# Kernel optimization log

Hardware: AMD Instinct MI355X
Metric: run time of the kernel (lower is better)

## Reference

```python
import jax, jax.numpy as jnp
import numpy as np

MARGIN1 = 0.3
MARGIN2 = 0.3
NUM_HARD_NEG = 10
CENTER_W = 0.01
NUM_CLASSES = 288
FEAT_DIM = 2048
N = 2048


def setup_inputs() -> dict:
    key = jax.random.key(0)
    k1, k2, k3 = jax.random.split(key, 3)
    embeddings = jax.random.normal(k1, (N, FEAT_DIM), dtype=jnp.float32)
    labels = jax.random.randint(k2, (N,), 0, NUM_CLASSES, dtype=jnp.int64)
    centers = jax.random.normal(k3, (NUM_CLASSES, FEAT_DIM), dtype=jnp.float32)
    return {"embeddings": embeddings, "labels": labels, "centers": centers}


def _pairwise_dist(x):
    # torch.cdist(x, x, p=2): Euclidean distance matrix [n, n]
    sq = jnp.sum(x * x, axis=1)
    d2 = sq[:, None] + sq[None, :] - 2.0 * (x @ x.T)
    return jnp.sqrt(jnp.maximum(d2, 1e-12))


def _quadruplet_loss(embeddings, centers, labels):
    n = embeddings.shape[0]
    dist = _pairwise_dist(embeddings)                      # [n, n]
    same = labels[:, None] == labels[None, :]
    eye = jnp.eye(n, dtype=bool)
    pos_mask = same & ~eye                                 # [n, n]
    neg_mask = ~same                                       # [n, n]

    # random positive per anchor (uniform over positives), fixed key
    u = jax.random.uniform(jax.random.key(42), (n, n))
    pos_idx = jnp.argmax(jnp.where(pos_mask, u, -1.0), axis=1)   # [n]
    has_pos = jnp.any(pos_mask, axis=1)
    neg_count = jnp.sum(neg_mask, axis=1)
    anchor_valid = has_pos & (neg_count >= 2)              # [n]

    # hard-negative mining: k smallest distances among negatives
    inf = jnp.asarray(jnp.inf, dist.dtype)
    masked = jnp.where(neg_mask, dist, inf)
    neg_d, negs1 = jax.lax.top_k(-masked, NUM_HARD_NEG)    # [n, k]
    d_an = -neg_d                                          # [n, k]

    # neg2: nearest negative (w.r.t. anchor's label set) to neg1, excluding neg1
    rows = dist[negs1]                                     # [n, k, n]
    excl = jnp.arange(n)[None, None, :] == negs1[:, :, None]
    cand = neg_mask[:, None, :] & ~excl                    # [n, k, n]
    d_n1n2 = jnp.min(jnp.where(cand, rows, inf), axis=2)   # [n, k]

    d_ap = dist[jnp.arange(n), pos_idx][:, None]           # [n, 1]

    valid = anchor_valid[:, None] & jnp.isfinite(d_an) & jnp.isfinite(d_n1n2)
    terms = (jax.nn.relu(d_ap - d_an + MARGIN1)
             + jax.nn.relu(d_ap - d_n1n2 + MARGIN2))       # [n, k]
    cnt = jnp.sum(valid)
    total = jnp.sum(jnp.where(valid, terms, 0.0))
    quad = jnp.where(cnt > 0, total / jnp.maximum(cnt, 1).astype(terms.dtype), 0.0)

    # center loss
    batch_centers = centers[labels]                        # [n, d]
    center = jnp.mean(jnp.sum((embeddings - batch_centers) ** 2, axis=1))
    return quad + CENTER_W * center


def reference(embeddings, labels, centers):
    return _quadruplet_loss(embeddings, centers, labels)
```

## Files before the change

kernel.cpp:

```cpp
#include <hip/hip_runtime.h>
#include <hip/hip_bf16.h>

#define N 2048
#define FEAT 2048
#define K_NEG 10
#define NCLS 288
#define M1 0.3f
#define M2 0.3f
#define CW 0.01f

#define BT 64
#define GT (N / BT)
#define NBLK (GT * (GT + 1) / 2)
#define BK 128
#define NT (FEAT / BK)

typedef __attribute__((ext_vector_type(8))) __bf16 bf16x8;
typedef __attribute__((ext_vector_type(4))) float f32x4;
typedef unsigned long long u64;

__device__ __forceinline__ unsigned short f32_to_bf16(float f) {
    unsigned int u = __float_as_uint(f);
    u += 0x7fffu + ((u >> 16) & 1u);
    return (unsigned short)(u >> 16);
}

__device__ __forceinline__ unsigned int rotl32(unsigned int x, int d) {
    return (x << d) | (x >> (32 - d));
}

__device__ __attribute__((noinline)) float threefry_uniform(unsigned int f) {
    const unsigned int H = (unsigned int)(N) * (unsigned int)(N) / 2u;
    unsigned int x0, x1; int word;
    if (f < H) { x0 = f;     x1 = f + H; word = 0; }
    else       { x0 = f - H; x1 = f;     word = 1; }
    unsigned int ks[3];
    ks[0] = 0u; ks[1] = 42u; ks[2] = 0u ^ 42u ^ 0x1BD11BDAu;
    x0 += ks[0]; x1 += ks[1];
    const int rotA[4] = {13, 15, 26, 6};
    const int rotB[4] = {17, 29, 16, 24};
    #pragma unroll
    for (int i = 0; i < 5; ++i) {
        const int* r = (i & 1) ? rotB : rotA;
        #pragma unroll
        for (int j = 0; j < 4; ++j) {
            x0 += x1; x1 = rotl32(x1, r[j]); x1 ^= x0;
        }
        x0 += ks[(i + 1) % 3];
        x1 += ks[(i + 2) % 3] + (unsigned int)(i + 1);
    }
    unsigned int bits = (word == 0) ? x0 : x1;
    return __uint_as_float((bits >> 9) | 0x3f800000u) - 1.0f;
}

__device__ __forceinline__ void gld16(const unsigned short* g, unsigned short* l) {
    __builtin_amdgcn_global_load_lds(
        (const __attribute__((address_space(1))) unsigned int*)g,
        (__attribute__((address_space(3))) unsigned int*)l,
        16, 0, 0);
}

__device__ __forceinline__ u64 shfl_xor_u64(u64 v, int mask) {
    unsigned int lo = (unsigned int)v, hi = (unsigned int)(v >> 32);
    lo = __shfl_xor(lo, mask);
    hi = __shfl_xor(hi, mask);
    return ((u64)hi << 32) | (u64)lo;
}

__global__ void __launch_bounds__(256) prep_kernel(
        const float* __restrict__ emb, const int* __restrict__ labels,
        const float* __restrict__ centers, unsigned short* __restrict__ xbf,
        float* __restrict__ sq, float* __restrict__ centerp) {
    int i = blockIdx.x;
    int t = threadIdx.x;
    int lab = labels[i];
    const float4* erow = (const float4*)(emb + (size_t)i * FEAT);
    const float4* crow = (const float4*)(centers + (size_t)lab * FEAT);
    uint2* xrow = (uint2*)(xbf + (size_t)i * FEAT);
    float ssum = 0.f, csum = 0.f;
    #pragma unroll
    for (int p = 0; p < 2; ++p) {
        int idx4 = p * 256 + t;
        float4 e = erow[idx4];
        float4 c = crow[idx4];
        ssum += e.x*e.x + e.y*e.y + e.z*e.z + e.w*e.w;
        float dx = e.x-c.x, dy = e.y-c.y, dz = e.z-c.z, dw = e.w-c.w;
        csum += dx*dx + dy*dy + dz*dz + dw*dw;
        unsigned int w0 = (unsigned int)f32_to_bf16(e.x) | ((unsigned int)f32_to_bf16(e.y) << 16);
        unsigned int w1 = (unsigned int)f32_to_bf16(e.z) | ((unsigned int)f32_to_bf16(e.w) << 16);
        xrow[idx4] = make_uint2(w0, w1);
    }
    #pragma unroll
    for (int off = 32; off; off >>= 1) {
        ssum += __shfl_xor(ssum, off);
        csum += __shfl_xor(csum, off);
    }
    __shared__ float s1[4], s2[4];
    int lane = t & 63, w = t >> 6;
    if (lane == 0) { s1[w] = ssum; s2[w] = csum; }
    __syncthreads();
    if (t == 0) {
        sq[i]      = s1[0] + s1[1] + s1[2] + s1[3];
        centerp[i] = s2[0] + s2[1] + s2[2] + s2[3];
    }
}

__global__ void __launch_bounds__(256) gemm_dist_kernel(
        const unsigned short* __restrict__ xbf, const float* __restrict__ sq,
        float* __restrict__ dist) {
    __shared__ __align__(16) unsigned short smem[4 * BT * BK];
    unsigned short (*As)[BT * BK] = (unsigned short(*)[BT * BK])smem;
    unsigned short (*Bs)[BT * BK] = (unsigned short(*)[BT * BK])(smem + 2 * BT * BK);
    float (*Ts)[68] = (float(*)[68])smem;

    int bid = blockIdx.x;
    int p = (bid & 7) * (NBLK / 8) + (bid >> 3);
    int by = 0, rem = p;
    while (rem >= GT - by) { rem -= GT - by; ++by; }
    int bx = by + rem;
    int brow0 = by * BT;
    int bcol0 = bx * BT;

    int t = threadIdx.x;
    int lane = t & 63, wid = t >> 6;
    int wr = wid >> 1, wc = wid & 1;
    f32x4 acc[2][2] = {};

    #define STAGE(buf, kelem) do {                                              \
        _Pragma("unroll")                                                       \
        for (int q = 0; q < 4; ++q) {                                           \
            int chunk = q * 256 + t;                                            \
            int row = chunk >> 4, c16 = chunk & 15;                             \
            int csrc = c16 ^ (row & 7);             \
            gld16(xbf + (size_t)(brow0 + row) * FEAT + (kelem) + csrc * 8,      \
                  &As[buf][chunk * 8]);                                         \
            gld16(xbf + (size_t)(bcol0 + row) * FEAT + (kelem) + csrc * 8,      \
                  &Bs[buf][chunk * 8]);                                         \
        } } while (0)

    STAGE(0, 0);

    for (int kt = 0; kt < NT; ++kt) {
        int cur = kt & 1;
        if (kt + 1 < NT) {
            STAGE(cur ^ 1, (kt + 1) * BK);
            asm volatile("s_waitcnt vmcnt(8)" ::: "memory");
        } else {
            asm volatile("s_waitcnt vmcnt(0)" ::: "memory");
        }
        __builtin_amdgcn_s_barrier();
        asm volatile("" ::: "memory");

        bf16x8 a[4][2], b[4][2];
        #pragma unroll
        for (int kk = 0; kk < 4; ++kk) {
            #pragma unroll
            for (int m = 0; m < 2; ++m) {
                int r = wr * 32 + m * 16 + (lane & 15);
                int slot = (kk * 4 + (lane >> 4)) ^ (r & 7);
                a[kk][m] = *(const bf16x8*)(&As[cur][r * BK + slot * 8]);
            }
            #pragma unroll
            for (int n = 0; n < 2; ++n) {
                int r = wc * 32 + n * 16 + (lane & 15);
                int slot = (kk * 4 + (lane >> 4)) ^ (r & 7);
                b[kk][n] = *(const bf16x8*)(&Bs[cur][r * BK + slot * 8]);
            }
        }
        #pragma unroll
        for (int m = 0; m < 2; ++m)
            #pragma unroll
            for (int n = 0; n < 2; ++n)
                #pragma unroll
                for (int kk = 0; kk < 4; ++kk)
                    acc[m][n] = __builtin_amdgcn_mfma_f32_16x16x32_bf16(a[kk][m], b[kk][n], acc[m][n], 0, 0, 0);

        asm volatile("" ::: "memory");
        __builtin_amdgcn_s_barrier();
        asm volatile("" ::: "memory");
    }
    #undef STAGE

    bool offdiag = (bx != by);
    #pragma unroll
    for (int m = 0; m < 2; ++m) {
        int lrow_base = wr * 32 + m * 16 + (lane >> 4) * 4;
        #pragma unroll
        for (int n = 0; n < 2; ++n) {
            int lcol = wc * 32 + n * 16 + (lane & 15);
            int gcol = bcol0 + lcol;
            float sqc = sq[gcol];
            #pragma unroll
            for (int r = 0; r < 4; ++r) {
                int lrow = lrow_base + r;
                int grow = brow0 + lrow;
                float d2 = sq[grow] + sqc - 2.0f * acc[m][n][r];
                float d = sqrtf(fmaxf(d2, 1e-12f));
                dist[(size_t)grow * N + gcol] = d;
                if (offdiag) Ts[lcol][lrow] = d;
            }
        }
    }
    asm volatile("s_waitcnt lgkmcnt(0)" ::: "memory");
    __builtin_amdgcn_s_barrier();
    asm volatile("" ::: "memory");
    if (offdiag) {
        int tr = t >> 2, seg = t & 3;
        float4* dst = (float4*)(dist + (size_t)(bcol0 + tr) * N + brow0 + seg * 16);
        const float* srow = &Ts[tr][seg * 16];
        #pragma unroll
        for (int x = 0; x < 4; ++x)
            dst[x] = *(const float4*)(srow + x * 4);
    }
}

__global__ void __launch_bounds__(256) topk_kernel(
        const float* __restrict__ dist, const int* __restrict__ labels,
        float* __restrict__ d_ap, int* __restrict__ avalid,
        int* __restrict__ negs1, float* __restrict__ d_an,
        float* __restrict__ rmin1, int* __restrict__ rc1, float* __restrict__ rmin2) {
    int t = threadIdx.x;
    int lane = t & 63, w = t >> 6;
    int i = blockIdx.x * 4 + w;
    int lab = labels[i];
    const float INF = __int_as_float(0x7f800000);

    __shared__ unsigned int mbuck[4][NCLS];
    for (int c = lane; c < NCLS; c += 64) mbuck[w][c] = 0x7f800000u;
    asm volatile("s_waitcnt lgkmcnt(0)" ::: "memory");

    const float4* drow = (const float4*)(dist + (size_t)i * N);
    const int4*   lrow = (const int4*)labels;

    unsigned int t0v = 0xFFFFFFFFu, t1v = 0xFFFFFFFFu, t2v = 0xFFFFFFFFu, t3v = 0xFFFFFFFFu;
    int t0j = 0, t1j = 0, t2j = 0, t3j = 0;
    float bestu = -1.0f; int bestj = 0;
    int negc = 0;

    #pragma unroll
    for (int it = 0; it < 8; ++it) {
        int idx4 = it * 64 + lane;
        float4 dv = drow[idx4];
        int4   lv = lrow[idx4];
        #pragma unroll
        for (int e = 0; e < 4; ++e) {
            float dd = (e == 0) ? dv.x : (e == 1) ? dv.y : (e == 2) ? dv.z : dv.w;
            int   lj = (e == 0) ? lv.x : (e == 1) ? lv.y : (e == 2) ? lv.z : lv.w;
            int j = idx4 * 4 + e;
            unsigned int db = __float_as_uint(dd);
            bool self = (j == i);
            if (!self && db < mbuck[w][lj]) atomicMin(&mbuck[w][lj], db);
            if (lj == lab) {
                if (!self) {
                    float u = threefry_uniform((unsigned int)(i * N + j));
                    if (u > bestu || (u == bestu && j < bestj)) { bestu = u; bestj = j; }
                }
            } else {
                negc++;
                if (db < t3v) {
                    bool lt2 = db < t2v, lt1 = db < t1v, lt0 = db < t0v;
                    t3v = lt2 ? t2v : db;   t3j = lt2 ? t2j : j;
                    unsigned int n2v = lt1 ? t1v : db; int n2j = lt1 ? t1j : j;
                    t2v = lt2 ? n2v : t2v;  t2j = lt2 ? n2j : t2j;
                    unsigned int n1v = lt0 ? t0v : db; int n1j = lt0 ? t0j : j;
                    t1v = lt1 ? n1v : t1v;  t1j = lt1 ? n1j : t1j;
                    t0v = lt0 ? db : t0v;   t0j = lt0 ? j : t0j;
                }
            }
        }
    }

    #pragma unroll
    for (int o = 1; o < 64; o <<= 1) {
        float ou = __shfl_xor(bestu, o);
        int   oj = __shfl_xor(bestj, o);
        negc += __shfl_xor(negc, o);
        if (ou > bestu || (ou == bestu && oj < bestj)) { bestu = ou; bestj = oj; }
    }
    if (lane == 0) {
        bool has_pos = (bestu >= 0.0f);
        avalid[i] = (has_pos && negc >= 2) ? 1 : 0;
        d_ap[i]   = has_pos ? dist[(size_t)i * N + bestj] : 0.0f;
    }

    #pragma unroll 1
    for (int r = 0; r < K_NEG; ++r) {
        u64 myk = ((u64)t0v << 32) | (unsigned int)t0j;
        u64 kmin = myk;
        #pragma unroll
        for (int o = 1; o < 64; o <<= 1) {
            u64 ok = shfl_xor_u64(kmin, o);
            if (ok < kmin) kmin = ok;
        }
        unsigned int hv = (unsigned int)(kmin >> 32);
        bool fin = hv < 0x7f800000u;
        if (lane == 0) {
            d_an[i * K_NEG + r]  = fin ? __uint_as_float(hv) : INF;
            negs1[i * K_NEG + r] = fin ? (int)(kmin & 0xFFFFFFFFu) : 0;
        }
        bool won = fin && (myk == kmin);
        if (won) {
            t0v = t1v; t0j = t1j; t1v = t2v; t1j = t2j; t2v = t3v; t2j = t3j;
            t3v = 0xFFFFFFFFu; t3j = 0;
        }
        if (__any(won && t0v == 0xFFFFFFFFu)) {
            if (won && t0v == 0xFFFFFFFFu) {
                u64 best = 0xFFFFFFFFFFFFFFFFull;
                #pragma unroll 1
                for (int it = 0; it < 8; ++it) {
                    int idx4 = it * 64 + lane;
                    float4 dv = drow[idx4];
                    int4   lv = lrow[idx4];
                    #pragma unroll
                    for (int e = 0; e < 4; ++e) {
                        float dd = (e == 0) ? dv.x : (e == 1) ? dv.y : (e == 2) ? dv.z : dv.w;
                        int   lj = (e == 0) ? lv.x : (e == 1) ? lv.y : (e == 2) ? lv.z : lv.w;
                        int j = idx4 * 4 + e;
                        unsigned int db = __float_as_uint(dd);
                        if (lj != lab && db < 0x7f800000u) {
                            u64 kq = ((u64)db << 32) | (unsigned int)j;
                            if (kq > myk && kq < best) best = kq;
                        }
                    }
                }
                t0v = (unsigned int)(best >> 32);
                t0j = (int)(best & 0xFFFFFFFFu);
            }
        }
    }

    asm volatile("s_waitcnt lgkmcnt(0)" ::: "memory");
    {
        float m1v = __uint_as_float(mbuck[w][lane]);
        int   c1v = lane;
        float m2v = INF;
        #pragma unroll
        for (int p = 1; p < 4; ++p) {
            float b = __uint_as_float(mbuck[w][lane + p * 64]);
            if (b < m1v) { m2v = m1v; m1v = b; c1v = lane + p * 64; }
            else         { m2v = fminf(m2v, b); }
        }
        if (lane < NCLS - 256) {
            float b = __uint_as_float(mbuck[w][lane + 256]);
            if (b < m1v) { m2v = m1v; m1v = b; c1v = lane + 256; }
            else         { m2v = fminf(m2v, b); }
        }
        #pragma unroll
        for (int o = 1; o < 64; o <<= 1) {
            float o1 = __shfl_xor(m1v, o);
            int   oc = __shfl_xor(c1v, o);
            float o2 = __shfl_xor(m2v, o);
            if (o1 < m1v) { m2v = fminf(m1v, o2); m1v = o1; c1v = oc; }
            else          { m2v = fminf(m2v, o1); }
        }
        if (lane == 0) { rmin1[i] = m1v; rc1[i] = c1v; rmin2[i] = m2v; }
    }
}

__global__ void __launch_bounds__(256) terms_kernel(
        const int* __restrict__ labels, const int* __restrict__ negs1,
        const float* __restrict__ d_an, const float* __restrict__ d_ap,
        const int* __restrict__ avalid, const float* __restrict__ rmin1,
        const int* __restrict__ rc1, const float* __restrict__ rmin2,
        float* __restrict__ terms, float* __restrict__ validf) {
    int task = blockIdx.x * 256 + threadIdx.x;
    if (task >= N * K_NEG) return;
    int i = task / K_NEG;
    int n1 = negs1[task];
    int lab = labels[i];
    const float INF = __int_as_float(0x7f800000);
    float dn2 = (rc1[n1] == lab) ? rmin2[n1] : rmin1[n1];
    float dan = d_an[task];
    float dap = d_ap[i];
    float t1 = fmaxf(dap - dan + M1, 0.0f);
    float t2 = fmaxf(dap - dn2 + M2, 0.0f);
    bool valid = (avalid[i] != 0) && (dan < INF) && (dn2 < INF);
    terms[task]  = valid ? (t1 + t2) : 0.0f;
    validf[task] = valid ? 1.0f : 0.0f;
}

__global__ void __launch_bounds__(256) finalize_kernel(
        const float* __restrict__ terms, const float* __restrict__ validf,
        const float* __restrict__ centerp, float* __restrict__ out) {
    int t = threadIdx.x;
    float ts = 0.f, vs = 0.f, cs = 0.f;
    for (int j = t * 4; j < N * K_NEG; j += 1024) {
        const float4 tv = *(const float4*)(terms + j);
        const float4 vv = *(const float4*)(validf + j);
        ts += tv.x + tv.y + tv.z + tv.w;
        vs += vv.x + vv.y + vv.z + vv.w;
    }
    for (int j = t; j < N; j += 256) cs += centerp[j];
    __shared__ float a[256], b[256], c[256];
    a[t] = ts; b[t] = vs; c[t] = cs;
    __syncthreads();
    for (int s = 128; s > 0; s >>= 1) {
        if (t < s) { a[t] += a[t + s]; b[t] += b[t + s]; c[t] += c[t + s]; }
        __syncthreads();
    }
    if (t == 0) {
        float quad = (b[0] > 0.0f) ? (a[0] / b[0]) : 0.0f;
        out[0] = quad + CW * (c[0] / (float)N);
    }
}

extern "C" void kernel_launch(void* const* d_in, const int* in_sizes, int n_in,
                              void* d_out, int out_size, void* d_ws, size_t ws_size,
                              hipStream_t stream) {
    const float* emb     = (const float*)d_in[0];
    const int*   labels  = (const int*)d_in[1];
    const float* centers = (const float*)d_in[2];
    float* out = (float*)d_out;

    char* ws = (char*)d_ws;
    unsigned short* xbf = (unsigned short*)ws;
    float* dist = (float*)(ws + (size_t)8 * 1024 * 1024);
    char* p = ws + (size_t)24 * 1024 * 1024;
    float* sq      = (float*)p; p += N * 4;
    float* centerp = (float*)p; p += N * 4;
    float* d_ap    = (float*)p; p += N * 4;
    int*   avalid  = (int*)p;   p += N * 4;
    float* rmin1   = (float*)p; p += N * 4;
    int*   rc1     = (int*)p;   p += N * 4;
    float* rmin2   = (float*)p; p += N * 4;
    int*   negs1   = (int*)p;   p += N * K_NEG * 4;
    float* d_an    = (float*)p; p += N * K_NEG * 4;
    float* terms   = (float*)p; p += N * K_NEG * 4;
    float* validf  = (float*)p; p += N * K_NEG * 4;

    prep_kernel<<<N, 256, 0, stream>>>(emb, labels, centers, xbf, sq, centerp);
    gemm_dist_kernel<<<NBLK, 256, 0, stream>>>(xbf, sq, dist);
    topk_kernel<<<N / 4, 256, 0, stream>>>(dist, labels, d_ap, avalid, negs1, d_an,
                                           rmin1, rc1, rmin2);
    terms_kernel<<<(N * K_NEG + 255) / 256, 256, 0, stream>>>(
        labels, negs1, d_an, d_ap, avalid, rmin1, rc1, rmin2, terms, validf);
    finalize_kernel<<<1, 256, 0, stream>>>(terms, validf, centerp, out);
}
```

Baseline: 68.26 us.

## Enlarge distance GEMM tile to 128x128 with two-phase transposed writeback

Raises the symmetric distance GEMM block tile from 64 to 128 and lowers the K step from 128 to 64, so each wave now accumulates a 4x4 grid of MFMA fragments. The goal is more data reuse per shared-memory load and fewer blocks. The transposed mirror write of off-diagonal tiles now goes through shared memory in two column-half phases, since the 128x128 float tile does not fit in the reused buffer at once. The cost is more accumulator registers, which may lower occupancy, and only 136 blocks, which may leave many of the 256 CUs idle.

```diff
diff --git a/kernel.cpp b/kernel.cpp
--- a/kernel.cpp
+++ b/kernel.cpp
@@ -9,10 +9,10 @@
 #define M2 0.3f
 #define CW 0.01f
 
-#define BT 64
+#define BT 128
 #define GT (N / BT)
 #define NBLK (GT * (GT + 1) / 2)
-#define BK 128
+#define BK 64
 #define NT (FEAT / BK)
 
 typedef __attribute__((ext_vector_type(8))) __bf16 bf16x8;
@@ -111,7 +111,7 @@
     __shared__ __align__(16) unsigned short smem[4 * BT * BK];
     unsigned short (*As)[BT * BK] = (unsigned short(*)[BT * BK])smem;
     unsigned short (*Bs)[BT * BK] = (unsigned short(*)[BT * BK])(smem + 2 * BT * BK);
-    float (*Ts)[68] = (float(*)[68])smem;
+    float (*Ts)[132] = (float(*)[132])smem;
 
     int bid = blockIdx.x;
     int p = (bid & 7) * (NBLK / 8) + (bid >> 3);
@@ -124,13 +124,13 @@
     int t = threadIdx.x;
     int lane = t & 63, wid = t >> 6;
     int wr = wid >> 1, wc = wid & 1;
-    f32x4 acc[2][2] = {};
+    f32x4 acc[4][4] = {};
 
     #define STAGE(buf, kelem) do {                                              \
         _Pragma("unroll")                                                       \
         for (int q = 0; q < 4; ++q) {                                           \
             int chunk = q * 256 + t;                                            \
-            int row = chunk >> 4, c16 = chunk & 15;                             \
+            int row = chunk >> 3, c16 = chunk & 7;                              \
             int csrc = c16 ^ (row & 7);             \
             gld16(xbf + (size_t)(brow0 + row) * FEAT + (kelem) + csrc * 8,      \
                   &As[buf][chunk * 8]);                                         \
@@ -151,29 +151,27 @@
         __builtin_amdgcn_s_barrier();
         asm volatile("" ::: "memory");
 
-        bf16x8 a[4][2], b[4][2];
-        #pragma unroll
-        for (int kk = 0; kk < 4; ++kk) {
+        #pragma unroll
+        for (int kk = 0; kk < 2; ++kk) {
+            bf16x8 a[4], b[4];
             #pragma unroll
-            for (int m = 0; m < 2; ++m) {
-                int r = wr * 32 + m * 16 + (lane & 15);
+            for (int m = 0; m < 4; ++m) {
+                int r = wr * 64 + m * 16 + (lane & 15);
                 int slot = (kk * 4 + (lane >> 4)) ^ (r & 7);
-                a[kk][m] = *(const bf16x8*)(&As[cur][r * BK + slot * 8]);
+                a[m] = *(const bf16x8*)(&As[cur][r * BK + slot * 8]);
             }
             #pragma unroll
-            for (int n = 0; n < 2; ++n) {
-                int r = wc * 32 + n * 16 + (lane & 15);
+            for (int n = 0; n < 4; ++n) {
+                int r = wc * 64 + n * 16 + (lane & 15);
                 int slot = (kk * 4 + (lane >> 4)) ^ (r & 7);
-                b[kk][n] = *(const bf16x8*)(&Bs[cur][r * BK + slot * 8]);
-            }
-        }
-        #pragma unroll
-        for (int m = 0; m < 2; ++m)
+                b[n] = *(const bf16x8*)(&Bs[cur][r * BK + slot * 8]);
+            }
             #pragma unroll
-            for (int n = 0; n < 2; ++n)
+            for (int m = 0; m < 4; ++m)
                 #pragma unroll
-                for (int kk = 0; kk < 4; ++kk)
-                    acc[m][n] = __builtin_amdgcn_mfma_f32_16x16x32_bf16(a[kk][m], b[kk][n], acc[m][n], 0, 0, 0);
+                for (int n = 0; n < 4; ++n)
+                    acc[m][n] = __builtin_amdgcn_mfma_f32_16x16x32_bf16(a[m], b[n], acc[m][n], 0, 0, 0);
+        }
 
         asm volatile("" ::: "memory");
         __builtin_amdgcn_s_barrier();
@@ -183,34 +181,49 @@
 
     bool offdiag = (bx != by);
     #pragma unroll
-    for (int m = 0; m < 2; ++m) {
-        int lrow_base = wr * 32 + m * 16 + (lane >> 4) * 4;
-        #pragma unroll
-        for (int n = 0; n < 2; ++n) {
-            int lcol = wc * 32 + n * 16 + (lane & 15);
-            int gcol = bcol0 + lcol;
+    for (int m = 0; m < 4; ++m) {
+        int lrow_base = wr * 64 + m * 16 + (lane >> 4) * 4;
+        #pragma unroll
+        for (int n = 0; n < 4; ++n) {
+            int gcol = bcol0 + wc * 64 + n * 16 + (lane & 15);
             float sqc = sq[gcol];
             #pragma unroll
             for (int r = 0; r < 4; ++r) {
-                int lrow = lrow_base + r;
-                int grow = brow0 + lrow;
+                int grow = brow0 + lrow_base + r;
                 float d2 = sq[grow] + sqc - 2.0f * acc[m][n][r];
                 float d = sqrtf(fmaxf(d2, 1e-12f));
                 dist[(size_t)grow * N + gcol] = d;
-                if (offdiag) Ts[lcol][lrow] = d;
-            }
-        }
-    }
-    asm volatile("s_waitcnt lgkmcnt(0)" ::: "memory");
-    __builtin_amdgcn_s_barrier();
-    asm volatile("" ::: "memory");
+                acc[m][n][r] = d;
+            }
+        }
+    }
+
     if (offdiag) {
-        int tr = t >> 2, seg = t & 3;
-        float4* dst = (float4*)(dist + (size_t)(bcol0 + tr) * N + brow0 + seg * 16);
-        const float* srow = &Ts[tr][seg * 16];
-        #pragma unroll
-        for (int x = 0; x < 4; ++x)
-            dst[x] = *(const float4*)(srow + x * 4);
+        #pragma unroll 1
+        for (int ph = 0; ph < 2; ++ph) {
+            __syncthreads();
+            if (wc == ph) {
+                #pragma unroll
+                for (int m = 0; m < 4; ++m) {
+                    int lrow_base = wr * 64 + m * 16 + (lane >> 4) * 4;
+                    #pragma unroll
+                    for (int n = 0; n < 4; ++n) {
+                        int ci = n * 16 + (lane & 15);
+                        #pragma unroll
+                        for (int r = 0; r < 4; ++r)
+                            Ts[ci][lrow_base + r] = acc[m][n][r];
+                    }
+                }
+            }
+            __syncthreads();
+            #pragma unroll
+            for (int q = 0; q < 8; ++q) {
+                int cid = q * 256 + t;
+                int tr = cid >> 5, seg = cid & 31;
+                float4 v = *(const float4*)(&Ts[tr][seg * 4]);
+                *(float4*)(dist + (size_t)(bcol0 + ph * 64 + tr) * N + brow0 + seg * 4) = v;
+            }
+        }
     }
 }
 
```

After: 71.08 us. +4.1%, slower.
